# Optimization experiments

Hardware: AMD Instinct MI355X
Metric: run time of the kernel (lower is better)

Reference implementation:

```python
import jax, jax.numpy as jnp
import numpy as np
from jax import lax

IN_FEATURES = 1024
CLASSES = 512
OUT_CHANNELS = 32
N = 4096
CONV1_OUT = 32
K = 3


def setup_inputs() -> dict:
    key = jax.random.key(0)
    ks = jax.random.split(key, 7)
    s_lin = 1.0 / np.sqrt(IN_FEATURES)
    s_c1 = 1.0 / np.sqrt(1 * K)
    s_c2 = 1.0 / np.sqrt(CONV1_OUT * K)
    return {
        "x": jax.random.normal(ks[0], (N, IN_FEATURES), dtype=jnp.float32),
        "W_w": jax.random.uniform(ks[1], (CLASSES, IN_FEATURES), jnp.float32, -s_lin, s_lin),
        "W_b": jax.random.uniform(ks[2], (CLASSES,), jnp.float32, -s_lin, s_lin),
        "conv1_w": jax.random.uniform(ks[3], (CONV1_OUT, 1, K), jnp.float32, -s_c1, s_c1),
        "conv1_b": jax.random.uniform(ks[4], (CONV1_OUT,), jnp.float32, -s_c1, s_c1),
        "conv2_w": jax.random.uniform(ks[5], (OUT_CHANNELS, CONV1_OUT, K), jnp.float32, -s_c2, s_c2),
        "conv2_b": jax.random.uniform(ks[6], (OUT_CHANNELS,), jnp.float32, -s_c2, s_c2),
    }


def _conv1d(x, w, b):
    # x: [N, C_in, L], w: [C_out, C_in, K], padding=1 (same)
    y = lax.conv_general_dilated(
        x, w, window_strides=(1,), padding=((1, 1),),
        dimension_numbers=("NCH", "OIH", "NCH"))
    return y + b[None, :, None]


def reference(x, W_w, W_b, conv1_w, conv1_b, conv2_w, conv2_b):
    # SelfAttention: h = x W^T + b  -> [N, CLASSES]
    h = x @ W_w.T + W_b
    # attention = softmax(tanh(h h^T), dim=1)  -> [N, N]
    scores = jnp.tanh(h @ h.T)
    attn = jax.nn.softmax(scores, axis=1)
    a = jnp.tanh(attn @ h)                     # [N, CLASSES]
    a = jax.nn.relu(a)
    # unsqueeze(-1).permute(0,2,1): [N, CLASSES] -> [N, 1, CLASSES]
    z = a[:, None, :]
    z = jax.nn.relu(_conv1d(z, conv1_w, conv1_b))   # [N, 32, CLASSES]
    z = jax.nn.relu(_conv1d(z, conv2_w, conv2_b))   # [N, OUT_CHANNELS, CLASSES]
    return jnp.transpose(z, (0, 2, 1))              # [N, CLASSES, OUT_CHANNELS]
```

## Files before the change

kernel.cpp:

```cpp
#include <hip/hip_runtime.h>

typedef __bf16 bf16_t;
typedef __bf16 bf16x8 __attribute__((ext_vector_type(8)));
typedef __bf16 bf16x4v __attribute__((ext_vector_type(4)));
typedef __bf16 bf16x2 __attribute__((ext_vector_type(2)));
typedef float f32x4 __attribute__((ext_vector_type(4)));

__device__ __forceinline__ float tanh_fast(float x) {
  float a = fabsf(x);
  float e = __expf(-2.f * a);
  float t = (1.f - e) * __builtin_amdgcn_rcpf(1.f + e);
  return copysignf(t, x);
}

__device__ __forceinline__ void gload16(const void* g, void* l) {
  __builtin_amdgcn_global_load_lds(
      (const __attribute__((address_space(1))) void*)g,
      (__attribute__((address_space(3))) void*)l, 16, 0, 0);
}

__global__ __launch_bounds__(256) void cast_all_k(const float* __restrict__ x,
                                                  const float* __restrict__ Ww,
                                                  const float* __restrict__ w2,
                                                  bf16_t* __restrict__ xb,
                                                  bf16_t* __restrict__ Wbf,
                                                  bf16_t* __restrict__ w2rg) {
  const int bid = blockIdx.x;
  const int tid = threadIdx.x;
  if (bid < 4096) {
    const int i = bid * 256 + tid;
    float4 v = ((const float4*)x)[i];
    bf16x4v o;
    o[0] = (bf16_t)v.x; o[1] = (bf16_t)v.y; o[2] = (bf16_t)v.z; o[3] = (bf16_t)v.w;
    ((bf16x4v*)xb)[i] = o;
  } else if (bid < 4608) {
    const int i = (bid - 4096) * 256 + tid;
    float4 v = ((const float4*)Ww)[i];
    bf16x4v o;
    o[0] = (bf16_t)v.x; o[1] = (bf16_t)v.y; o[2] = (bf16_t)v.z; o[3] = (bf16_t)v.w;
    ((bf16x4v*)Wbf)[i] = o;
  } else {
    for (int i = tid; i < 3072; i += 256) {
      int o = i / 96, rem = i % 96, c = rem / 3, kk = rem % 3;
      w2rg[kk * 1024 + o * 32 + c] = (bf16_t)w2[i];
    }
  }
}

__global__ __launch_bounds__(256) void gemm1_fused_k(const bf16_t* __restrict__ xb,
                                                     const bf16_t* __restrict__ Wbf,
                                                     const float* __restrict__ bias,
                                                     bf16_t* __restrict__ h,
                                                     bf16_t* __restrict__ hT) {
  __shared__ bf16_t As[64 * 32];
  __shared__ bf16_t Bs[128 * 32];
  __shared__ bf16_t tileO[64][136];
  const int tid = threadIdx.x;
  const int w = tid >> 6, l = tid & 63;
  const int lr = l & 15, lkq = l >> 4;
  const int bx = blockIdx.x, by = blockIdx.y;

  const bf16_t* Ag  = xb + (size_t)(by * 64 + (tid >> 2)) * 1024 + (tid & 3) * 8;
  const bf16_t* Bg0 = Wbf + (size_t)(bx * 128 + (tid >> 2)) * 1024 + (tid & 3) * 8;
  const bf16_t* Bg1 = Bg0 + (size_t)64 * 1024;
  bf16_t* lA  = As + tid * 8;
  bf16_t* lB0 = Bs + tid * 8;
  bf16_t* lB1 = Bs + 2048 + tid * 8;

  f32x4 acc[4][2];
#pragma unroll
  for (int m = 0; m < 4; ++m)
#pragma unroll
    for (int n = 0; n < 2; ++n) acc[m][n] = (f32x4){0.f, 0.f, 0.f, 0.f};

  for (int kt = 0; kt < 1024; kt += 32) {
    gload16(Ag + kt, lA);
    gload16(Bg0 + kt, lB0);
    gload16(Bg1 + kt, lB1);
    __syncthreads();
    bf16x8 af[4], bfv[2];
#pragma unroll
    for (int m = 0; m < 4; ++m)
      af[m] = *(const bf16x8*)&As[(m * 16 + lr) * 32 + lkq * 8];
#pragma unroll
    for (int n = 0; n < 2; ++n)
      bfv[n] = *(const bf16x8*)&Bs[(w * 32 + n * 16 + lr) * 32 + lkq * 8];
#pragma unroll
    for (int m = 0; m < 4; ++m)
#pragma unroll
      for (int n = 0; n < 2; ++n)
        acc[m][n] = __builtin_amdgcn_mfma_f32_16x16x32_bf16(af[m], bfv[n], acc[m][n], 0, 0, 0);
    __syncthreads();
  }

  float bcol[2];
#pragma unroll
  for (int n = 0; n < 2; ++n) bcol[n] = bias[bx * 128 + w * 32 + n * 16 + lr];

#pragma unroll
  for (int m = 0; m < 4; ++m)
#pragma unroll
    for (int v = 0; v < 4; ++v) {
      const int r = m * 16 + lkq * 4 + v;
#pragma unroll
      for (int n = 0; n < 2; ++n)
        tileO[r][w * 32 + n * 16 + lr] = (bf16_t)(acc[m][n][v] + bcol[n]);
    }
  __syncthreads();

#pragma unroll
  for (int k = 0; k < 4; ++k) {
    const int idx = k * 256 + tid;
    const int row = idx >> 4, vec = idx & 15;
    bf16x8 vv = *(const bf16x8*)&tileO[row][vec * 8];
    *(bf16x8*)&h[(size_t)(by * 64 + row) * 512 + bx * 128 + vec * 8] = vv;
  }
#pragma unroll
  for (int k = 0; k < 4; ++k) {
    const int idx = k * 256 + tid;
    const int d = idx >> 3, vec = idx & 7;
    bf16x8 u;
#pragma unroll
    for (int e = 0; e < 8; ++e) u[e] = tileO[vec * 8 + e][d];
    *(bf16x8*)&hT[(size_t)(bx * 128 + d) * 4096 + by * 64 + vec * 8] = u;
  }
}

#define BAR() __builtin_amdgcn_s_barrier()
#define WLG() asm volatile("s_waitcnt lgkmcnt(0)" ::: "memory")
#define RDA(b, am)                                                              \
  do {                                                                          \
    _Pragma("unroll") for (int j = 0; j < 4; ++j) {                             \
      afr[j][0] = *(const bf16x8*)(pA + (b)*16384 + (am)*4096 + j*1024);        \
      afr[j][1] = *(const bf16x8*)(pA + (b)*16384 + 8192 + (am)*4096 + j*1024); \
    }                                                                           \
  } while (0)
#define RDB(b, bn)                                                              \
  do {                                                                          \
    _Pragma("unroll") for (int jj = 0; jj < 2; ++jj) {                          \
      bfr[jj][0] = *(const bf16x8*)(pB + (b)*16384 + ((bn)*2+jj)*1024);         \
      bfr[jj][1] = *(const bf16x8*)(pB + (b)*16384 + 8192 + ((bn)*2+jj)*1024);  \
    }                                                                           \
  } while (0)
#define MM16(am, bn)                                                            \
  do {                                                                          \
    __builtin_amdgcn_s_setprio(1);                                              \
    _Pragma("unroll") for (int kk = 0; kk < 2; ++kk)                            \
    _Pragma("unroll") for (int j = 0; j < 4; ++j)                               \
    _Pragma("unroll") for (int jj = 0; jj < 2; ++jj)                            \
      acc[(am)*4+j][(bn)*2+jj] = __builtin_amdgcn_mfma_f32_16x16x32_bf16(       \
          afr[j][kk], bfr[jj][kk], acc[(am)*4+j][(bn)*2+jj], 0, 0, 0);          \
    __builtin_amdgcn_s_setprio(0);                                              \
  } while (0)
#define STGA(tile, half)                                                        \
  do {                                                                          \
    const bf16_t* s_ = Ag + (size_t)(half)*128*lda + (tile)*64;                 \
    char* d_ = lds_raw + (half)*32768 + ((tile)&1)*16384 + tid*16;              \
    gload16(s_, d_); gload16(s_ + 32, d_ + 8192);                               \
  } while (0)
#define STGB(tile, half)                                                        \
  do {                                                                          \
    const bf16_t* s_ = Bg + (size_t)(half)*128*ldb + (tile)*64;                 \
    char* d_ = lds_raw + 65536 + (half)*32768 + ((tile)&1)*16384 + tid*16;      \
    gload16(s_, d_); gload16(s_ + 32, d_ + 8192);                               \
  } while (0)

template <int EPI>
__global__ __launch_bounds__(512, 2) void gemm8_k(const bf16_t* __restrict__ A,
                                                  const bf16_t* __restrict__ Bt,
                                                  bf16_t* __restrict__ out,
                                                  float* __restrict__ psum,
                                                  int lda, int ldb, int ldc,
                                                  int Klen, size_t pstride) {
  __shared__ __attribute__((aligned(16))) char lds_raw[131072];
  const int tid = threadIdx.x;
  const int wid = tid >> 6, l = tid & 63;
  const int wm = wid >> 2, wn = wid & 3;
  const int lr = l & 15, lkq = l >> 4;

  const int gx = gridDim.x, gy = gridDim.y;
  const int flat = blockIdx.x + gx * (blockIdx.y + gy * blockIdx.z);
  const int n = gx * gy * gridDim.z;
  const int s = (flat & 7) * (n >> 3) + (flat >> 3);
  const int lgx = __builtin_ctz(gx), lgy = __builtin_ctz(gy);
  const int bx = s & (gx - 1);
  const int by = (s >> lgx) & (gy - 1);
  const int bz = s >> (lgx + lgy);

  const size_t koff = (size_t)bz * Klen;
  const int NI = Klen >> 7;

  const int srow = tid >> 2;
  const int scol = ((tid & 3) * 8) ^ (((tid >> 5) & 1) << 4);
  const bf16_t* Ag = A + (size_t)(by * 256 + srow) * lda + koff + scol;
  const bf16_t* Bg = Bt + (size_t)(bx * 256 + srow) * ldb + koff + scol;

  const int kby = (lkq * 16) ^ (((lr >> 3) & 1) << 5);
  const char* pA = lds_raw + wm * 32768 + lr * 64 + kby;
  const char* pB = lds_raw + 65536 + (wn >> 1) * 32768 + ((wn & 1) * 64 + lr) * 64 + kby;

  bf16x8 afr[4][2], bfr[2][2];
  f32x4 acc[8][4];
#pragma unroll
  for (int m = 0; m < 8; ++m)
#pragma unroll
    for (int n2 = 0; n2 < 4; ++n2) acc[m][n2] = (f32x4){0.f, 0.f, 0.f, 0.f};

  STGA(0, 0); STGA(0, 1); STGB(0, 0); STGB(0, 1); STGA(1, 0);

  for (int i = 0; i < NI; ++i) {
    const int t1 = 2 * i + 1, t2 = 2 * i + 2, t3 = 2 * i + 3;
    const bool more = (i + 1 < NI);
    asm volatile("s_waitcnt vmcnt(2)" ::: "memory");
    BAR();
    RDA(0, 0); RDB(0, 0);
    STGA(t1, 1);
    WLG(); MM16(0, 0); BAR();
    RDB(0, 1); STGB(t1, 0);
    BAR(); WLG(); MM16(0, 1); BAR();
    RDA(0, 1); STGB(t1, 1);
    BAR(); WLG(); MM16(1, 1); BAR();
    RDB(0, 0);
    if (more) STGA(t2, 0);
    BAR(); WLG(); MM16(1, 0); BAR();
    if (more) { asm volatile("s_waitcnt vmcnt(2)" ::: "memory"); }
    else      { asm volatile("s_waitcnt vmcnt(0)" ::: "memory"); }
    BAR();
    RDA(1, 0); RDB(1, 0);
    if (more) STGA(t2, 1);
    WLG(); MM16(0, 0); BAR();
    RDB(1, 1);
    if (more) STGB(t2, 0);
    BAR(); WLG(); MM16(0, 1); BAR();
    RDA(1, 1);
    if (more) STGB(t2, 1);
    BAR(); WLG(); MM16(1, 1); BAR();
    RDB(1, 0);
    if (more) STGA(t3, 0);
    BAR(); WLG(); MM16(1, 0); BAR();
  }

  if constexpr (EPI == 1) {
    float* ps = psum + (size_t)(bx * 4 + wn) * 4096;
#pragma unroll
    for (int mi = 0; mi < 8; ++mi) {
#pragma unroll
      for (int v = 0; v < 4; ++v) {
        const int r = wm * 128 + mi * 16 + lkq * 4 + v;
        float rs = 0.f;
#pragma unroll
        for (int ni = 0; ni < 4; ++ni) {
          float val = __expf(tanh_fast(acc[mi][ni][v]));
          const int cb = ((wn * 64 + ni * 16 + lr) * 2) ^ ((r & 4) << 4);
          *(bf16_t*)(lds_raw + r * 512 + cb) = (bf16_t)val;
          rs += val;
        }
        rs += __shfl_xor(rs, 1);
        rs += __shfl_xor(rs, 2);
        rs += __shfl_xor(rs, 4);
        rs += __shfl_xor(rs, 8);
        if (lr == 0) ps[by * 256 + r] = rs;
      }
    }
  } else {
#pragma unroll
    for (int mi = 0; mi < 8; ++mi)
#pragma unroll
      for (int v = 0; v < 4; ++v) {
        const int r = wm * 128 + mi * 16 + lkq * 4 + v;
#pragma unroll
        for (int ni = 0; ni < 4; ++ni) {
          const int cb = ((wn * 64 + ni * 16 + lr) * 2) ^ ((r & 4) << 4);
          *(bf16_t*)(lds_raw + r * 512 + cb) = (bf16_t)acc[mi][ni][v];
        }
      }
  }
  __syncthreads();
  bf16_t* obase = (EPI == 1) ? out : out + (size_t)bz * pstride;
#pragma unroll
  for (int k = 0; k < 16; ++k) {
    const int idx = k * 512 + tid;
    const int row = idx >> 5, cc = idx & 31;
    bf16x8 vv = *(const bf16x8*)(lds_raw + ((row * 512 + cc * 16) ^ ((row & 4) << 4)));
    *(bf16x8*)&obase[(size_t)(by * 256 + row) * ldc + bx * 256 + cc * 8] = vv;
  }
}

template <int EPI>
__global__ __launch_bounds__(256) void gemm_bt_k(const bf16_t* __restrict__ A,
                                                 const bf16_t* __restrict__ Bt,
                                                 const float* __restrict__ extra,
                                                 bf16_t* __restrict__ out,
                                                 float* __restrict__ outf,
                                                 float* __restrict__ psum,
                                                 int M, int N, int Kloop, int lda, int ldb) {
  __shared__ bf16_t As[128 * 32];
  __shared__ bf16_t Bs[128 * 32];
  const int tid = threadIdx.x;
  const int w = tid >> 6;
  const int l = tid & 63;
  const int bx = blockIdx.x, by = blockIdx.y;
  const int koff = blockIdx.z * Kloop;

  const bf16_t* src = (w < 2) ? A : Bt;
  const int stride = (w < 2) ? lda : ldb;
  bf16_t* dstbase = (w < 2) ? As : Bs;
  const int tile0 = (w < 2 ? by : bx) * 128 + (w & 1) * 64;
  const int srow = l >> 2;
  const int scol = (l & 3) * 8;
  const bf16_t* gbase = src + (size_t)(tile0 + srow) * stride + scol + koff;
  bf16_t* lbase = dstbase + (w & 1) * (64 * 32);

  const int wm = w >> 1, wn = w & 1;
  const int lrow = l & 15;
  const int lk = (l >> 4) * 8;

  f32x4 zero = {0.f, 0.f, 0.f, 0.f};
  f32x4 acc[4][4];
  for (int m = 0; m < 4; ++m)
    for (int n = 0; n < 4; ++n) acc[m][n] = zero;

  for (int kt = 0; kt < Kloop; kt += 32) {
    const bf16_t* g = gbase + kt;
#pragma unroll
    for (int i = 0; i < 4; ++i) gload16(g + (size_t)i * 16 * stride, lbase + i * 512);
    __syncthreads();
    bf16x8 af[4], bfv[4];
#pragma unroll
    for (int m = 0; m < 4; ++m)
      af[m] = *(const bf16x8*)&As[(wm * 64 + m * 16 + lrow) * 32 + lk];
#pragma unroll
    for (int n = 0; n < 4; ++n)
      bfv[n] = *(const bf16x8*)&Bs[(wn * 64 + n * 16 + lrow) * 32 + lk];
#pragma unroll
    for (int m = 0; m < 4; ++m)
#pragma unroll
      for (int n = 0; n < 4; ++n)
        acc[m][n] = __builtin_amdgcn_mfma_f32_16x16x32_bf16(af[m], bfv[n], acc[m][n], 0, 0, 0);
    __syncthreads();
  }

  const int row0 = by * 128 + wm * 64;
  const int col0 = bx * 128 + wn * 64;

  if constexpr (EPI == 3) {
    float* of = outf + (size_t)blockIdx.z * M * N;
#pragma unroll
    for (int m = 0; m < 4; ++m)
#pragma unroll
      for (int v = 0; v < 4; ++v) {
        const int row = row0 + m * 16 + ((l >> 4) << 2) + v;
#pragma unroll
        for (int n = 0; n < 4; ++n)
          of[(size_t)row * N + col0 + n * 16 + lrow] = acc[m][n][v];
      }
    return;
  }

  if constexpr (EPI == 1) {
#pragma unroll
    for (int m = 0; m < 4; ++m)
#pragma unroll
      for (int v = 0; v < 4; ++v) {
        const int row = row0 + m * 16 + ((l >> 4) << 2) + v;
        float rs = 0.f;
#pragma unroll
        for (int n = 0; n < 4; ++n) {
          const int col = col0 + n * 16 + lrow;
          float val = __expf(tanh_fast(acc[m][n][v]));
          out[(size_t)row * N + col] = (bf16_t)val;
          rs += val;
        }
        if (psum) {
          rs += __shfl_xor(rs, 1);
          rs += __shfl_xor(rs, 2);
          rs += __shfl_xor(rs, 4);
          rs += __shfl_xor(rs, 8);
          if ((l & 15) == 0) psum[(size_t)(bx * 2 + wn) * M + row] = rs;
        }
      }
    return;
  }

  float bcol[4];
#pragma unroll
  for (int n = 0; n < 4; ++n)
    bcol[n] = (EPI == 0) ? extra[col0 + n * 16 + lrow] : 0.f;

#pragma unroll
  for (int m = 0; m < 4; ++m) {
#pragma unroll
    for (int v = 0; v < 4; ++v) {
      const int row = row0 + m * 16 + ((l >> 4) << 2) + v;
      float inv_dn = 1.f;
      if constexpr (EPI == 2) inv_dn = 1.f / extra[row];
#pragma unroll
      for (int n = 0; n < 4; ++n) {
        const int col = col0 + n * 16 + lrow;
        float val = acc[m][n][v];
        float o;
        if constexpr (EPI == 0) o = val + bcol[n];
        else o = fmaxf(tanh_fast(val * inv_dn), 0.f);
        out[(size_t)row * N + col] = (bf16_t)o;
      }
    }
  }
}

__global__ __launch_bounds__(256) void transpose_k(const bf16_t* __restrict__ h,
                                                   bf16_t* __restrict__ hT) {
  __shared__ bf16_t tile[64][65];
  const int i0 = blockIdx.x * 64;
  const int d0 = blockIdx.y * 64;
  const int tid = threadIdx.x;
#pragma unroll
  for (int p = 0; p < 2; ++p) {
    int r = p * 32 + (tid >> 3);
    int c8 = (tid & 7) * 8;
    bf16x8 v = *(const bf16x8*)&h[(size_t)(i0 + r) * 512 + d0 + c8];
#pragma unroll
    for (int k = 0; k < 8; ++k) tile[r][c8 + k] = v[k];
  }
  __syncthreads();
#pragma unroll
  for (int p = 0; p < 2; ++p) {
    int d = p * 32 + (tid >> 3);
    int i8 = (tid & 7) * 8;
    bf16x8 u;
#pragma unroll
    for (int k = 0; k < 8; ++k) u[k] = tile[i8 + k][d];
    *(bf16x8*)&hT[(size_t)(d0 + d) * 4096 + i0 + i8] = u;
  }
}

__global__ __launch_bounds__(256) void rowsum_k(const bf16_t* __restrict__ P,
                                                float* __restrict__ den) {
  const int r = blockIdx.x;
  const int tid = threadIdx.x;
  const bf16_t* p = P + (size_t)r * 4096 + tid * 16;
  bf16x8 a = *(const bf16x8*)p;
  bf16x8 b = *(const bf16x8*)(p + 8);
  float s = 0.f;
#pragma unroll
  for (int k = 0; k < 8; ++k) s += (float)a[k] + (float)b[k];
  __shared__ float red[256];
  red[tid] = s;
  __syncthreads();
  for (int off = 128; off > 0; off >>= 1) {
    if (tid < off) red[tid] += red[tid + off];
    __syncthreads();
  }
  if (tid == 0) den[r] = red[0];
}

__global__ __launch_bounds__(256) void conv2_fused_k(const bf16_t* __restrict__ pg,
                                                     const float* __restrict__ psum,
                                                     const bf16_t* __restrict__ w2rg,
                                                     const float* __restrict__ w1,
                                                     const float* __restrict__ b1,
                                                     const float* __restrict__ b2,
                                                     float* __restrict__ out, int S) {
  __shared__ bf16_t trow[516];
  __shared__ bf16_t z1t[514 * 40];
  __shared__ bf16_t w2r[3072];
  __shared__ float w1s[96], b1s[32], b2s[32];
  __shared__ float den_s;
  const int r = blockIdx.x;
  const int tid = threadIdx.x;

  if (tid < 96) w1s[tid] = w1[tid];
  if (tid < 32) { b1s[tid] = b1[tid]; b2s[tid] = b2[tid]; }
  ((bf16x8*)w2r)[tid] = ((const bf16x8*)w2rg)[tid];
  if (tid < 128) ((bf16x8*)w2r)[256 + tid] = ((const bf16x8*)w2rg)[256 + tid];

  if (tid < 64) {
    float dp = psum[(size_t)tid * 4096 + r];
    dp += __shfl_xor(dp, 32);
    dp += __shfl_xor(dp, 16);
    dp += __shfl_xor(dp, 8);
    dp += __shfl_xor(dp, 4);
    dp += __shfl_xor(dp, 2);
    dp += __shfl_xor(dp, 1);
    if (tid == 0) den_s = dp;
  }

  float a0 = 0.f, a1 = 0.f;
  {
    const bf16_t* pr = pg + (size_t)r * 512 + tid * 2;
    for (int z = 0; z < S; ++z) {
      bf16x2 v = *(const bf16x2*)(pr + (size_t)z * (4096 * 512));
      a0 += (float)v[0];
      a1 += (float)v[1];
    }
  }
  if (tid == 0) { trow[0] = (bf16_t)0.f; trow[513] = (bf16_t)0.f; }
  if (tid < 40) { z1t[tid] = (bf16_t)0.f; z1t[513 * 40 + tid] = (bf16_t)0.f; }
  __syncthreads();

  {
    const float inv = 1.f / den_s;
    trow[1 + 2 * tid] = (bf16_t)fmaxf(tanh_fast(a0 * inv), 0.f);
    trow[2 + 2 * tid] = (bf16_t)fmaxf(tanh_fast(a1 * inv), 0.f);
  }
  __syncthreads();

  {
    const int c = tid & 31;
    const int jb = (tid >> 5) * 64;
    const float wc0 = w1s[c * 3], wc1 = w1s[c * 3 + 1], wc2 = w1s[c * 3 + 2];
    const float bb = b1s[c];
    float tm = (float)trow[jb];
    float t0 = (float)trow[jb + 1];
    for (int j = jb; j < jb + 64; ++j) {
      float tp2 = (float)trow[j + 2];
      float v = fmaxf(bb + wc0 * tm + wc1 * t0 + wc2 * tp2, 0.f);
      z1t[(j + 1) * 40 + c] = (bf16_t)v;
      tm = t0; t0 = tp2;
    }
  }
  __syncthreads();

  const int w = tid >> 6, l = tid & 63;
  const int lrow = l & 15;
  const int lk = (l >> 4) * 8;
  bf16x8 af[3][2];
#pragma unroll
  for (int kk = 0; kk < 3; ++kk)
#pragma unroll
    for (int m = 0; m < 2; ++m)
      af[kk][m] = *(const bf16x8*)&w2r[kk * 1024 + (m * 16 + lrow) * 32 + lk];

  f32x4 zero = {0.f, 0.f, 0.f, 0.f};
  f32x4 acc[2][8];
#pragma unroll
  for (int m = 0; m < 2; ++m)
#pragma unroll
    for (int n = 0; n < 8; ++n) acc[m][n] = zero;

  const int j0 = w * 128;
#pragma unroll
  for (int kk = 0; kk < 3; ++kk) {
#pragma unroll
    for (int n = 0; n < 8; ++n) {
      bf16x8 bfv = *(const bf16x8*)&z1t[(j0 + n * 16 + lrow + kk) * 40 + lk];
      acc[0][n] = __builtin_amdgcn_mfma_f32_16x16x32_bf16(af[kk][0], bfv, acc[0][n], 0, 0, 0);
      acc[1][n] = __builtin_amdgcn_mfma_f32_16x16x32_bf16(af[kk][1], bfv, acc[1][n], 0, 0, 0);
    }
  }

#pragma unroll
  for (int m = 0; m < 2; ++m) {
    const int ob = m * 16 + ((l >> 4) << 2);
    const float bb0 = b2s[ob], bb1 = b2s[ob + 1], bb2 = b2s[ob + 2], bb3 = b2s[ob + 3];
#pragma unroll
    for (int n = 0; n < 8; ++n) {
      const int j = j0 + n * 16 + lrow;
      f32x4 res;
      res[0] = fmaxf(acc[m][n][0] + bb0, 0.f);
      res[1] = fmaxf(acc[m][n][1] + bb1, 0.f);
      res[2] = fmaxf(acc[m][n][2] + bb2, 0.f);
      res[3] = fmaxf(acc[m][n][3] + bb3, 0.f);
      *(f32x4*)&out[((size_t)r * 512 + j) * 32 + ob] = res;
    }
  }
}

__global__ __launch_bounds__(256) void conv_fused_k(const bf16_t* __restrict__ t,
                                                    const float* __restrict__ w1,
                                                    const float* __restrict__ b1,
                                                    const float* __restrict__ w2,
                                                    const float* __restrict__ b2,
                                                    float* __restrict__ out) {
  __shared__ bf16_t trow[516];
  __shared__ bf16_t z1t[514 * 40];
  __shared__ bf16_t w2r[3 * 32 * 32];
  __shared__ float w1s[96], b1s[32], b2s[32];
  const int r = blockIdx.x;
  const int tid = threadIdx.x;

  if (tid < 96) w1s[tid] = w1[tid];
  if (tid < 32) { b1s[tid] = b1[tid]; b2s[tid] = b2[tid]; }
  for (int i = tid; i < 3072; i += 256) {
    int o = i / 96, rem = i % 96, c = rem / 3, kk = rem % 3;
    w2r[kk * 1024 + o * 32 + c] = (bf16_t)w2[i];
  }
  {
    const bf16_t* tp = t + (size_t)r * 512;
    trow[1 + tid] = tp[tid];
    trow[1 + 256 + tid] = tp[256 + tid];
    if (tid == 0) { trow[0] = (bf16_t)0.f; trow[513] = (bf16_t)0.f; }
    if (tid < 40) { z1t[tid] = (bf16_t)0.f; z1t[513 * 40 + tid] = (bf16_t)0.f; }
  }
  __syncthreads();

  {
    const int c = tid & 31;
    const int jb = (tid >> 5) * 64;
    const float wc0 = w1s[c * 3], wc1 = w1s[c * 3 + 1], wc2 = w1s[c * 3 + 2];
    const float bb = b1s[c];
    float tm = (float)trow[jb];
    float t0 = (float)trow[jb + 1];
    for (int j = jb; j < jb + 64; ++j) {
      float tp2 = (float)trow[j + 2];
      float v = fmaxf(bb + wc0 * tm + wc1 * t0 + wc2 * tp2, 0.f);
      z1t[(j + 1) * 40 + c] = (bf16_t)v;
      tm = t0; t0 = tp2;
    }
  }
  __syncthreads();

  const int w = tid >> 6, l = tid & 63;
  const int lrow = l & 15;
  const int lk = (l >> 4) * 8;
  bf16x8 af[3][2];
#pragma unroll
  for (int kk = 0; kk < 3; ++kk)
#pragma unroll
    for (int m = 0; m < 2; ++m)
      af[kk][m] = *(const bf16x8*)&w2r[kk * 1024 + (m * 16 + lrow) * 32 + lk];

  f32x4 zero = {0.f, 0.f, 0.f, 0.f};
  f32x4 acc[2][8];
#pragma unroll
  for (int m = 0; m < 2; ++m)
#pragma unroll
    for (int n = 0; n < 8; ++n) acc[m][n] = zero;

  const int j0 = w * 128;
#pragma unroll
  for (int kk = 0; kk < 3; ++kk) {
#pragma unroll
    for (int n = 0; n < 8; ++n) {
      bf16x8 bfv = *(const bf16x8*)&z1t[(j0 + n * 16 + lrow + kk) * 40 + lk];
      acc[0][n] = __builtin_amdgcn_mfma_f32_16x16x32_bf16(af[kk][0], bfv, acc[0][n], 0, 0, 0);
      acc[1][n] = __builtin_amdgcn_mfma_f32_16x16x32_bf16(af[kk][1], bfv, acc[1][n], 0, 0, 0);
    }
  }

#pragma unroll
  for (int m = 0; m < 2; ++m) {
    const int ob = m * 16 + ((l >> 4) << 2);
    const float bb0 = b2s[ob], bb1 = b2s[ob + 1], bb2 = b2s[ob + 2], bb3 = b2s[ob + 3];
#pragma unroll
    for (int n = 0; n < 8; ++n) {
      const int j = j0 + n * 16 + lrow;
      f32x4 res;
      res[0] = fmaxf(acc[m][n][0] + bb0, 0.f);
      res[1] = fmaxf(acc[m][n][1] + bb1, 0.f);
      res[2] = fmaxf(acc[m][n][2] + bb2, 0.f);
      res[3] = fmaxf(acc[m][n][3] + bb3, 0.f);
      *(f32x4*)&out[((size_t)r * 512 + j) * 32 + ob] = res;
    }
  }
}

extern "C" void kernel_launch(void* const* d_in, const int* in_sizes, int n_in,
                              void* d_out, int out_size, void* d_ws, size_t ws_size,
                              hipStream_t stream) {
  const float* x = (const float*)d_in[0];
  const float* Ww = (const float*)d_in[1];
  const float* Wb = (const float*)d_in[2];
  const float* c1w = (const float*)d_in[3];
  const float* c1b = (const float*)d_in[4];
  const float* c2w = (const float*)d_in[5];
  const float* c2b = (const float*)d_in[6];
  float* out = (float*)d_out;
  char* ws = (char*)d_ws;

  bf16_t* xb  = (bf16_t*)(ws + 0);
  bf16_t* Wbf = (bf16_t*)(ws + 8388608);
  bf16_t* h   = (bf16_t*)(ws + 9437184);
  bf16_t* hT  = (bf16_t*)(ws + 13631488);
  bf16_t* tb  = (bf16_t*)(ws + 17825792);
  bf16_t* w2rg = (bf16_t*)(ws + 17825792);
  float*  den = (float*)(ws + 22020096);

  cast_all_k<<<4609, 256, 0, stream>>>(x, Ww, c2w, xb, Wbf, w2rg);

  const size_t NEED_FAST = 73416704ull;
  if (ws_size >= NEED_FAST) {
    float*  psum = (float*)(ws + 22036480);
    bf16_t* P    = (bf16_t*)(ws + 23085056);
    bf16_t* pg3b = (bf16_t*)(ws + 56639488);

    gemm1_fused_k<<<dim3(4, 64), 256, 0, stream>>>(xb, Wbf, Wb, h, hT);

    gemm8_k<1><<<dim3(16, 16, 1), 512, 0, stream>>>(h, h, P, psum, 512, 512, 4096, 512, 0);

    const int S = (ws_size >= 90193920ull) ? 8 : 4;
    gemm8_k<3><<<dim3(2, 16, S), 512, 0, stream>>>(P, hT, pg3b, nullptr, 4096, 4096, 512,
                                                   4096 / S, (size_t)4096 * 512);

    conv2_fused_k<<<4096, 256, 0, stream>>>(pg3b, psum, w2rg, c1w, c1b, c2b, out, S);
  } else {
    bf16_t* P = (bf16_t*)(ws + 22036480);
    gemm_bt_k<0><<<dim3(4, 32), 256, 0, stream>>>(xb, Wbf, Wb, h, nullptr, nullptr,
                                                  4096, 512, 1024, 1024, 1024);
    transpose_k<<<dim3(64, 8), 256, 0, stream>>>(h, hT);
    gemm_bt_k<1><<<dim3(32, 32), 256, 0, stream>>>(h, h, nullptr, P, nullptr, nullptr,
                                                   4096, 4096, 512, 512, 512);
    rowsum_k<<<4096, 256, 0, stream>>>(P, den);
    gemm_bt_k<2><<<dim3(4, 32), 256, 0, stream>>>(P, hT, den, tb, nullptr, nullptr,
                                                  4096, 512, 4096, 4096, 4096);
    conv_fused_k<<<4096, 256, 0, stream>>>(tb, c1w, c1b, c2w, c2b, out);
  }
}
```

Before: 181.2 us.

## Fuse x bf16 cast into gemm1 and split conv epilogue rows across two blocks

The x-to-bf16 cast pass is removed from the fast path. gemm1 now loads fp32 x directly, converts it in registers and writes the bf16 tile to LDS, while a smaller kernel casts only the weights. This removes a 16MB read and 8MB write round trip. The conv epilogue kernel now splits each row into two 256-column halves with a 2-element halo, doubling the block count and halving LDS per block for higher occupancy, at the cost of some duplicated halo work and replacing the async LDS load of the A operand with synchronous register loads.

```diff
diff --git a/kernel.cpp b/kernel.cpp
--- a/kernel.cpp
+++ b/kernel.cpp
@@ -17,6 +17,26 @@
   __builtin_amdgcn_global_load_lds(
       (const __attribute__((address_space(1))) void*)g,
       (__attribute__((address_space(3))) void*)l, 16, 0, 0);
+}
+
+__global__ __launch_bounds__(256) void cast_w_k(const float* __restrict__ Ww,
+                                                const float* __restrict__ w2,
+                                                bf16_t* __restrict__ Wbf,
+                                                bf16_t* __restrict__ w2rg) {
+  const int bid = blockIdx.x;
+  const int tid = threadIdx.x;
+  if (bid < 512) {
+    const int i = bid * 256 + tid;
+    float4 v = ((const float4*)Ww)[i];
+    bf16x4v o;
+    o[0] = (bf16_t)v.x; o[1] = (bf16_t)v.y; o[2] = (bf16_t)v.z; o[3] = (bf16_t)v.w;
+    ((bf16x4v*)Wbf)[i] = o;
+  } else {
+    for (int i = tid; i < 3072; i += 256) {
+      int o = i / 96, rem = i % 96, c = rem / 3, kk = rem % 3;
+      w2rg[kk * 1024 + o * 32 + c] = (bf16_t)w2[i];
+    }
+  }
 }
 
 __global__ __launch_bounds__(256) void cast_all_k(const float* __restrict__ x,
@@ -47,7 +67,7 @@
   }
 }
 
-__global__ __launch_bounds__(256) void gemm1_fused_k(const bf16_t* __restrict__ xb,
+__global__ __launch_bounds__(256) void gemm1_fused_k(const float* __restrict__ x,
                                                      const bf16_t* __restrict__ Wbf,
                                                      const float* __restrict__ bias,
                                                      bf16_t* __restrict__ h,
@@ -60,7 +80,7 @@
   const int lr = l & 15, lkq = l >> 4;
   const int bx = blockIdx.x, by = blockIdx.y;
 
-  const bf16_t* Ag  = xb + (size_t)(by * 64 + (tid >> 2)) * 1024 + (tid & 3) * 8;
+  const float* Ax   = x + (size_t)(by * 64 + (tid >> 2)) * 1024 + (tid & 3) * 8;
   const bf16_t* Bg0 = Wbf + (size_t)(bx * 128 + (tid >> 2)) * 1024 + (tid & 3) * 8;
   const bf16_t* Bg1 = Bg0 + (size_t)64 * 1024;
   bf16_t* lA  = As + tid * 8;
@@ -74,9 +94,14 @@
     for (int n = 0; n < 2; ++n) acc[m][n] = (f32x4){0.f, 0.f, 0.f, 0.f};
 
   for (int kt = 0; kt < 1024; kt += 32) {
-    gload16(Ag + kt, lA);
+    float4 xa = *(const float4*)(Ax + kt);
+    float4 xc = *(const float4*)(Ax + kt + 4);
     gload16(Bg0 + kt, lB0);
     gload16(Bg1 + kt, lB1);
+    bf16x8 av;
+    av[0] = (bf16_t)xa.x; av[1] = (bf16_t)xa.y; av[2] = (bf16_t)xa.z; av[3] = (bf16_t)xa.w;
+    av[4] = (bf16_t)xc.x; av[5] = (bf16_t)xc.y; av[6] = (bf16_t)xc.z; av[7] = (bf16_t)xc.w;
+    *(bf16x8*)lA = av;
     __syncthreads();
     bf16x8 af[4], bfv[2];
 #pragma unroll
@@ -453,19 +478,21 @@
   if (tid == 0) den[r] = red[0];
 }
 
-__global__ __launch_bounds__(256) void conv2_fused_k(const bf16_t* __restrict__ pg,
-                                                     const float* __restrict__ psum,
-                                                     const bf16_t* __restrict__ w2rg,
-                                                     const float* __restrict__ w1,
-                                                     const float* __restrict__ b1,
-                                                     const float* __restrict__ b2,
-                                                     float* __restrict__ out, int S) {
-  __shared__ bf16_t trow[516];
-  __shared__ bf16_t z1t[514 * 40];
+__global__ __launch_bounds__(256, 4) void conv2_fused_k(const bf16_t* __restrict__ pg,
+                                                        const float* __restrict__ psum,
+                                                        const bf16_t* __restrict__ w2rg,
+                                                        const float* __restrict__ w1,
+                                                        const float* __restrict__ b1,
+                                                        const float* __restrict__ b2,
+                                                        float* __restrict__ out, int S) {
+  __shared__ bf16_t trow[264];
+  __shared__ bf16_t z1t[258 * 40 + 8];
   __shared__ bf16_t w2r[3072];
   __shared__ float w1s[96], b1s[32], b2s[32];
   __shared__ float den_s;
-  const int r = blockIdx.x;
+  const int r = blockIdx.x >> 1;
+  const int half = blockIdx.x & 1;
+  const int j0 = half * 256;
   const int tid = threadIdx.x;
 
   if (tid < 96) w1s[tid] = w1[tid];
@@ -486,21 +513,124 @@
 
   float a0 = 0.f, a1 = 0.f;
   {
-    const bf16_t* pr = pg + (size_t)r * 512 + tid * 2;
-    for (int z = 0; z < S; ++z) {
-      bf16x2 v = *(const bf16x2*)(pr + (size_t)z * (4096 * 512));
-      a0 += (float)v[0];
-      a1 += (float)v[1];
-    }
-  }
-  if (tid == 0) { trow[0] = (bf16_t)0.f; trow[513] = (bf16_t)0.f; }
-  if (tid < 40) { z1t[tid] = (bf16_t)0.f; z1t[513 * 40 + tid] = (bf16_t)0.f; }
+    const int jA = j0 - 2 + tid;
+    if (jA >= 0 && jA < 512) {
+      const bf16_t* pr = pg + (size_t)r * 512 + jA;
+      for (int z = 0; z < S; ++z) a0 += (float)pr[(size_t)z * (4096 * 512)];
+    }
+    if (tid < 4) {
+      const int jB = j0 - 2 + 256 + tid;
+      if (jB >= 0 && jB < 512) {
+        const bf16_t* pr = pg + (size_t)r * 512 + jB;
+        for (int z = 0; z < S; ++z) a1 += (float)pr[(size_t)z * (4096 * 512)];
+      }
+    }
+  }
   __syncthreads();
 
   {
     const float inv = 1.f / den_s;
-    trow[1 + 2 * tid] = (bf16_t)fmaxf(tanh_fast(a0 * inv), 0.f);
-    trow[2 + 2 * tid] = (bf16_t)fmaxf(tanh_fast(a1 * inv), 0.f);
+    const int jA = j0 - 2 + tid;
+    trow[tid] = (jA >= 0 && jA < 512) ? (bf16_t)fmaxf(tanh_fast(a0 * inv), 0.f)
+                                      : (bf16_t)0.f;
+    if (tid < 4) {
+      const int jB = j0 - 2 + 256 + tid;
+      trow[256 + tid] = (jB >= 0 && jB < 512) ? (bf16_t)fmaxf(tanh_fast(a1 * inv), 0.f)
+                                              : (bf16_t)0.f;
+    }
+  }
+  __syncthreads();
+
+  {
+    const int c = tid & 31;
+    const int g = tid >> 5;
+    const int mb = g * 33;
+    const int me = (mb + 33 < 258) ? mb + 33 : 258;
+    const float wc0 = w1s[c * 3], wc1 = w1s[c * 3 + 1], wc2 = w1s[c * 3 + 2];
+    const float bb = b1s[c];
+    float tm = (float)trow[mb];
+    float t0 = (float)trow[mb + 1];
+    for (int m = mb; m < me; ++m) {
+      float tp2 = (float)trow[m + 2];
+      float v = fmaxf(bb + wc0 * tm + wc1 * t0 + wc2 * tp2, 0.f);
+      const int jp = j0 - 1 + m;
+      if (jp < 0 || jp > 511) v = 0.f;
+      z1t[m * 40 + c] = (bf16_t)v;
+      tm = t0; t0 = tp2;
+    }
+  }
+  __syncthreads();
+
+  const int w = tid >> 6, l = tid & 63;
+  const int lrow = l & 15;
+  const int lk = (l >> 4) * 8;
+  bf16x8 af[3][2];
+#pragma unroll
+  for (int kk = 0; kk < 3; ++kk)
+#pragma unroll
+    for (int m = 0; m < 2; ++m)
+      af[kk][m] = *(const bf16x8*)&w2r[kk * 1024 + (m * 16 + lrow) * 32 + lk];
+
+  f32x4 zero = {0.f, 0.f, 0.f, 0.f};
+  f32x4 acc[2][4];
+#pragma unroll
+  for (int m = 0; m < 2; ++m)
+#pragma unroll
+    for (int n = 0; n < 4; ++n) acc[m][n] = zero;
+
+  const int jlb = w * 64;
+#pragma unroll
+  for (int kk = 0; kk < 3; ++kk) {
+#pragma unroll
+    for (int n = 0; n < 4; ++n) {
+      bf16x8 bfv = *(const bf16x8*)&z1t[(jlb + n * 16 + lrow + kk) * 40 + lk];
+      acc[0][n] = __builtin_amdgcn_mfma_f32_16x16x32_bf16(af[kk][0], bfv, acc[0][n], 0, 0, 0);
+      acc[1][n] = __builtin_amdgcn_mfma_f32_16x16x32_bf16(af[kk][1], bfv, acc[1][n], 0, 0, 0);
+    }
+  }
+
+#pragma unroll
+  for (int m = 0; m < 2; ++m) {
+    const int ob = m * 16 + ((l >> 4) << 2);
+    const float bb0 = b2s[ob], bb1 = b2s[ob + 1], bb2 = b2s[ob + 2], bb3 = b2s[ob + 3];
+#pragma unroll
+    for (int n = 0; n < 4; ++n) {
+      const int j = j0 + jlb + n * 16 + lrow;
+      f32x4 res;
+      res[0] = fmaxf(acc[m][n][0] + bb0, 0.f);
+      res[1] = fmaxf(acc[m][n][1] + bb1, 0.f);
+      res[2] = fmaxf(acc[m][n][2] + bb2, 0.f);
+      res[3] = fmaxf(acc[m][n][3] + bb3, 0.f);
+      *(f32x4*)&out[((size_t)r * 512 + j) * 32 + ob] = res;
+    }
+  }
+}
+
+__global__ __launch_bounds__(256) void conv_fused_k(const bf16_t* __restrict__ t,
+                                                    const float* __restrict__ w1,
+                                                    const float* __restrict__ b1,
+                                                    const float* __restrict__ w2,
+                                                    const float* __restrict__ b2,
+                                                    float* __restrict__ out) {
+  __shared__ bf16_t trow[516];
+  __shared__ bf16_t z1t[514 * 40];
+  __shared__ bf16_t w2r[3 * 32 * 32];
+  __shared__ float w1s[96], b1s[32], b2s[32];
+  const int r = blockIdx.x;
+  const int tid = threadIdx.x;
+
+  if (tid < 96) w1s[tid] = w1[tid];
+  if (tid < 32) { b1s[tid] = b1[tid]; b2s[tid] = b2[tid]; }
+  for (int i = tid; i < 3072; i += 256) {
+    int o = i / 96, rem = i % 96, c = rem / 3, kk = rem % 3;
+    w2r[kk * 1024 + o * 32 + c] = (bf16_t)w2[i];
+  }
+  {
+    const bf16_t* tp = t + (size_t)r * 512;
+    trow[1 + tid] = tp[tid];
+    trow[1 + 256 + tid] = tp[256 + tid];
+    if (tid == 0) { trow[0] = (bf16_t)0.f; trow[513] = (bf16_t)0.f; }
+    if (tid < 40) { z1t[tid] = (bf16_t)0.f; z1t[513 * 40 + tid] = (bf16_t)0.f; }
   }
   __syncthreads();
 
@@ -565,95 +695,6 @@
   }
 }
 
-__global__ __launch_bounds__(256) void conv_fused_k(const bf16_t* __restrict__ t,
-                                                    const float* __restrict__ w1,
-                                                    const float* __restrict__ b1,
-                                                    const float* __restrict__ w2,
-                                                    const float* __restrict__ b2,
-                                                    float* __restrict__ out) {
-  __shared__ bf16_t trow[516];
-  __shared__ bf16_t z1t[514 * 40];
-  __shared__ bf16_t w2r[3 * 32 * 32];
-  __shared__ float w1s[96], b1s[32], b2s[32];
-  const int r = blockIdx.x;
-  const int tid = threadIdx.x;
-
-  if (tid < 96) w1s[tid] = w1[tid];
-  if (tid < 32) { b1s[tid] = b1[tid]; b2s[tid] = b2[tid]; }
-  for (int i = tid; i < 3072; i += 256) {
-    int o = i / 96, rem = i % 96, c = rem / 3, kk = rem % 3;
-    w2r[kk * 1024 + o * 32 + c] = (bf16_t)w2[i];
-  }
-  {
-    const bf16_t* tp = t + (size_t)r * 512;
-    trow[1 + tid] = tp[tid];
-    trow[1 + 256 + tid] = tp[256 + tid];
-    if (tid == 0) { trow[0] = (bf16_t)0.f; trow[513] = (bf16_t)0.f; }
-    if (tid < 40) { z1t[tid] = (bf16_t)0.f; z1t[513 * 40 + tid] = (bf16_t)0.f; }
-  }
-  __syncthreads();
-
-  {
-    const int c = tid & 31;
-    const int jb = (tid >> 5) * 64;
-    const float wc0 = w1s[c * 3], wc1 = w1s[c * 3 + 1], wc2 = w1s[c * 3 + 2];
-    const float bb = b1s[c];
-    float tm = (float)trow[jb];
-    float t0 = (float)trow[jb + 1];
-    for (int j = jb; j < jb + 64; ++j) {
-      float tp2 = (float)trow[j + 2];
-      float v = fmaxf(bb + wc0 * tm + wc1 * t0 + wc2 * tp2, 0.f);
-      z1t[(j + 1) * 40 + c] = (bf16_t)v;
-      tm = t0; t0 = tp2;
-    }
-  }
-  __syncthreads();
-
-  const int w = tid >> 6, l = tid & 63;
-  const int lrow = l & 15;
-  const int lk = (l >> 4) * 8;
-  bf16x8 af[3][2];
-#pragma unroll
-  for (int kk = 0; kk < 3; ++kk)
-#pragma unroll
-    for (int m = 0; m < 2; ++m)
-      af[kk][m] = *(const bf16x8*)&w2r[kk * 1024 + (m * 16 + lrow) * 32 + lk];
-
-  f32x4 zero = {0.f, 0.f, 0.f, 0.f};
-  f32x4 acc[2][8];
-#pragma unroll
-  for (int m = 0; m < 2; ++m)
-#pragma unroll
-    for (int n = 0; n < 8; ++n) acc[m][n] = zero;
-
-  const int j0 = w * 128;
-#pragma unroll
-  for (int kk = 0; kk < 3; ++kk) {
-#pragma unroll
-    for (int n = 0; n < 8; ++n) {
-      bf16x8 bfv = *(const bf16x8*)&z1t[(j0 + n * 16 + lrow + kk) * 40 + lk];
-      acc[0][n] = __builtin_amdgcn_mfma_f32_16x16x32_bf16(af[kk][0], bfv, acc[0][n], 0, 0, 0);
-      acc[1][n] = __builtin_amdgcn_mfma_f32_16x16x32_bf16(af[kk][1], bfv, acc[1][n], 0, 0, 0);
-    }
-  }
-
-#pragma unroll
-  for (int m = 0; m < 2; ++m) {
-    const int ob = m * 16 + ((l >> 4) << 2);
-    const float bb0 = b2s[ob], bb1 = b2s[ob + 1], bb2 = b2s[ob + 2], bb3 = b2s[ob + 3];
-#pragma unroll
-    for (int n = 0; n < 8; ++n) {
-      const int j = j0 + n * 16 + lrow;
-      f32x4 res;
-      res[0] = fmaxf(acc[m][n][0] + bb0, 0.f);
-      res[1] = fmaxf(acc[m][n][1] + bb1, 0.f);
-      res[2] = fmaxf(acc[m][n][2] + bb2, 0.f);
-      res[3] = fmaxf(acc[m][n][3] + bb3, 0.f);
-      *(f32x4*)&out[((size_t)r * 512 + j) * 32 + ob] = res;
-    }
-  }
-}
-
 extern "C" void kernel_launch(void* const* d_in, const int* in_sizes, int n_in,
                               void* d_out, int out_size, void* d_ws, size_t ws_size,
                               hipStream_t stream) {
@@ -675,15 +716,15 @@
   bf16_t* w2rg = (bf16_t*)(ws + 17825792);
   float*  den = (float*)(ws + 22020096);
 
-  cast_all_k<<<4609, 256, 0, stream>>>(x, Ww, c2w, xb, Wbf, w2rg);
-
   const size_t NEED_FAST = 73416704ull;
   if (ws_size >= NEED_FAST) {
     float*  psum = (float*)(ws + 22036480);
     bf16_t* P    = (bf16_t*)(ws + 23085056);
     bf16_t* pg3b = (bf16_t*)(ws + 56639488);
 
-    gemm1_fused_k<<<dim3(4, 64), 256, 0, stream>>>(xb, Wbf, Wb, h, hT);
+    cast_w_k<<<513, 256, 0, stream>>>(Ww, c2w, Wbf, w2rg);
+
+    gemm1_fused_k<<<dim3(4, 64), 256, 0, stream>>>(x, Wbf, Wb, h, hT);
 
     gemm8_k<1><<<dim3(16, 16, 1), 512, 0, stream>>>(h, h, P, psum, 512, 512, 4096, 512, 0);
 
@@ -691,9 +732,10 @@
     gemm8_k<3><<<dim3(2, 16, S), 512, 0, stream>>>(P, hT, pg3b, nullptr, 4096, 4096, 512,
                                                    4096 / S, (size_t)4096 * 512);
 
-    conv2_fused_k<<<4096, 256, 0, stream>>>(pg3b, psum, w2rg, c1w, c1b, c2b, out, S);
+    conv2_fused_k<<<8192, 256, 0, stream>>>(pg3b, psum, w2rg, c1w, c1b, c2b, out, S);
   } else {
     bf16_t* P = (bf16_t*)(ws + 22036480);
+    cast_all_k<<<4609, 256, 0, stream>>>(x, Ww, c2w, xb, Wbf, w2rg);
     gemm_bt_k<0><<<dim3(4, 32), 256, 0, stream>>>(xb, Wbf, Wb, h, nullptr, nullptr,
                                                   4096, 512, 1024, 1024, 1024);
     transpose_k<<<dim3(64, 8), 256, 0, stream>>>(h, hT);
```

Measured after the change: 188.4 us. 4.0% more time.
